# Performance work log

Measured on AMD Instinct MI355X. Metric: run time of the kernel, lower is better.

The kernel has to match this reference:

```python
import jax, jax.numpy as jnp
import numpy as np

HEADS = 8
DIM_HEAD = 64
SCALE = DIM_HEAD ** -0.5


def setup_inputs() -> dict:
    key = jax.random.key(0)
    ks = jax.random.split(key, 7)
    B, N, Dq = 2, 4096, 512
    M, Dc = 4096, 768
    inner = HEADS * DIM_HEAD  # 512
    x = jax.random.normal(ks[0], (B, N, Dq), dtype=jnp.float32)
    context = jax.random.normal(ks[1], (B, M, Dc), dtype=jnp.float32)
    # weights stored [in, out] (torch Linear weight transposed)
    Wq = jax.random.normal(ks[2], (Dq, inner), dtype=jnp.float32) * (Dq ** -0.5)
    Wk = jax.random.normal(ks[3], (Dc, inner), dtype=jnp.float32) * (Dc ** -0.5)
    Wv = jax.random.normal(ks[4], (Dc, inner), dtype=jnp.float32) * (Dc ** -0.5)
    Wo = jax.random.normal(ks[5], (inner, Dq), dtype=jnp.float32) * (inner ** -0.5)
    bo = jax.random.normal(ks[6], (Dq,), dtype=jnp.float32) * 0.01
    return {"x": x, "context": context, "Wq": Wq, "Wk": Wk, "Wv": Wv, "Wo": Wo, "bo": bo}


def reference(x, context, Wq, Wk, Wv, Wo, bo):
    B, N, _ = x.shape
    M = context.shape[1]
    h, d = HEADS, DIM_HEAD
    q = (x @ Wq).reshape(B, N, h, d)                      # b n h d
    k = ((context @ Wk) * SCALE).reshape(B, M, h, d)      # scale applied to k, as in source
    v = (context @ Wv).reshape(B, M, h, d)
    scores = jnp.einsum('bnhd,bmhd->bhnm', q, k)          # full QK^T
    attn = jax.nn.softmax(scores, axis=-1)
    out = jnp.einsum('bhnm,bmhd->bnhd', attn, v).reshape(B, N, h * d)
    return out @ Wo + bo  # dropout p=0.0 -> identity
```

## Files before the change

kernel.cpp:

```cpp
#include <hip/hip_runtime.h>

typedef unsigned short u16;
typedef __attribute__((ext_vector_type(4))) unsigned short u16x4;
typedef __attribute__((ext_vector_type(8))) unsigned short u16x8;
typedef __attribute__((ext_vector_type(8))) short s16x8;
typedef __attribute__((ext_vector_type(4))) float f32x4;
typedef __attribute__((ext_vector_type(16))) float f32x16;
typedef __attribute__((ext_vector_type(4))) unsigned int u32x4;

#define LOG2E 1.4426950408889634f

__device__ __forceinline__ u16 f2bf(float f) {
    return __builtin_bit_cast(unsigned short, static_cast<__bf16>(f));
}

__device__ __forceinline__ float fexp2(float x) {
#if __has_builtin(__builtin_amdgcn_exp2f)
    return __builtin_amdgcn_exp2f(x);
#else
    return exp2f(x);
#endif
}

__device__ __forceinline__ s16x8 ld_frag(const u16* p) {
    return __builtin_bit_cast(s16x8, *reinterpret_cast<const u16x8*>(p));
}

__device__ __forceinline__ f32x4 mfma16(s16x8 a, s16x8 b, f32x4 c) {
    return __builtin_amdgcn_mfma_f32_16x16x32_bf16(a, b, c, 0, 0, 0);
}

__device__ __forceinline__ f32x16 mfma32(s16x8 a, s16x8 b, f32x16 c) {
    return __builtin_amdgcn_mfma_f32_32x32x16_bf16(a, b, c, 0, 0, 0);
}

__device__ __forceinline__ unsigned cvt_pk_bf16(float lo, float hi2) {
    unsigned r;
    asm("v_cvt_pk_bf16_f32 %0, %1, %2" : "=v"(r) : "v"(lo), "v"(hi2));
    return r;
}

__device__ __forceinline__ void plane32_swap(unsigned& x, unsigned& y) {
#if __has_builtin(__builtin_amdgcn_permlane32_swap)
    auto r = __builtin_amdgcn_permlane32_swap(x, y, false, false);
    x = r[0];
    y = r[1];
#else
    asm("v_permlane32_swap_b32 %0, %1" : "+v"(x), "+v"(y));
#endif
}

__device__ __forceinline__ void async16(const u16* g, u16* lds) {
    __builtin_amdgcn_global_load_lds(
        (__attribute__((address_space(1))) void*)const_cast<u16*>(g),
        (__attribute__((address_space(3))) void*)lds, 16, 0, 0);
}

__global__ __launch_bounds__(256) void cvt_bf16_kernel(const float* __restrict__ in,
                                                       u16* __restrict__ out, int n8) {
    int i = blockIdx.x * 256 + threadIdx.x;
    if (i >= n8) return;
    const f32x4* p = (const f32x4*)in + ((size_t)i << 1);
    f32x4 a = p[0], c = p[1];
    u16x8 v;
    v[0] = f2bf(a[0]); v[1] = f2bf(a[1]); v[2] = f2bf(a[2]); v[3] = f2bf(a[3]);
    v[4] = f2bf(c[0]); v[5] = f2bf(c[1]); v[6] = f2bf(c[2]); v[7] = f2bf(c[3]);
    *((u16x8*)out + i) = v;
}

__global__ __launch_bounds__(256) void wtrans_kernel(const float* __restrict__ W,
                                                     u16* __restrict__ Wt, int Kd, float scale) {
    __shared__ float t[32][33];
    const int k0 = blockIdx.x << 5, n0 = blockIdx.y << 5;
    const int tx = threadIdx.x, ty = threadIdx.y;
#pragma unroll
    for (int i = 0; i < 32; i += 8)
        t[ty + i][tx] = W[(size_t)(k0 + ty + i) * 512 + n0 + tx] * scale;
    __syncthreads();
#pragma unroll
    for (int i = 0; i < 32; i += 8)
        Wt[(size_t)(n0 + ty + i) * Kd + k0 + tx] = f2bf(t[tx][ty + i]);
}

__global__ __launch_bounds__(256) void vtrans_kernel(const u16* __restrict__ Vb,
                                                     u16* __restrict__ Vt) {
    __shared__ u16 t[64][72];
    const int bh = blockIdx.y, m0 = blockIdx.x << 6;
    const int b = bh >> 3, h = bh & 7;
    const int tid = threadIdx.x;
#pragma unroll
    for (int i = 0; i < 2; i++) {
        int f = tid + i * 256, r = f >> 3, sg = f & 7;
        u16x8 v = *(const u16x8*)(Vb + (size_t)(b * 4096 + m0 + r) * 512 + (h << 6) + (sg << 3));
        *(u16x8*)&t[r][sg << 3] = v;
    }
    __syncthreads();
#pragma unroll
    for (int i = 0; i < 2; i++) {
        int f = tid + i * 256, dr = f >> 3, sg = f & 7;
        u16x8 v;
#pragma unroll
        for (int j = 0; j < 8; j++) v[j] = t[(sg << 3) + j][dr];
        *(u16x8*)(Vt + (size_t)bh * 262144 + (size_t)dr * 4096 + m0 + (sg << 3)) = v;
    }
}

template <bool BF16OUT>
__device__ __forceinline__ void gemm_body(const u16* __restrict__ A, const u16* __restrict__ Bt,
                                          void* __restrict__ Cv, const float* __restrict__ bias,
                                          int K) {
    __shared__ u16 Ab[2][128 * 64];
    __shared__ u16 Bb[2][128 * 64];
    const int tid = threadIdx.x;
    const int w = tid >> 6, l = tid & 63;
    const int lg = l >> 4, lq = l & 15;
    const int wm = w >> 1, wn = w & 1;
    const int bm = blockIdx.y, bn = blockIdx.x;
    const int KT = K >> 6;

    f32x4 acc[4][4];
#pragma unroll
    for (int i = 0; i < 4; i++)
#pragma unroll
        for (int j = 0; j < 4; j++) acc[i][j] = (f32x4){0.f, 0.f, 0.f, 0.f};

    const u16* Ag0 = A + (size_t)bm * 128 * K;
    const u16* Bg0 = Bt + (size_t)bn * 128 * K;
    const int srow = l >> 3, scol = (l & 7) << 3;

    auto stage = [&](int kt, int buf) {
#pragma unroll
        for (int i = 0; i < 4; i++) {
            const int c = (w << 2) + i;
            const int row = (c << 3) + srow;
            async16(Ag0 + (size_t)row * K + kt * 64 + scol, &Ab[buf][c << 9]);
            async16(Bg0 + (size_t)row * K + kt * 64 + scol, &Bb[buf][c << 9]);
        }
    };

    stage(0, 0);
    for (int kt = 0; kt < KT; ++kt) {
        __syncthreads();
        if (kt + 1 < KT) stage(kt + 1, (kt + 1) & 1);
        const u16* As = Ab[kt & 1];
        const u16* Bs = Bb[kt & 1];
#pragma unroll
        for (int s = 0; s < 2; s++) {
            s16x8 af[4], bfr[4];
#pragma unroll
            for (int mt = 0; mt < 4; mt++)
                af[mt] = ld_frag(As + ((wm << 6) + (mt << 4) + lq) * 64 + (s << 5) + (lg << 3));
#pragma unroll
            for (int nt = 0; nt < 4; nt++)
                bfr[nt] = ld_frag(Bs + ((wn << 6) + (nt << 4) + lq) * 64 + (s << 5) + (lg << 3));
#pragma unroll
            for (int mt = 0; mt < 4; mt++)
#pragma unroll
                for (int nt = 0; nt < 4; nt++)
                    acc[mt][nt] = mfma16(af[mt], bfr[nt], acc[mt][nt]);
        }
    }
    const int row0 = bm * 128 + (wm << 6);
    const int col0 = bn * 128 + (wn << 6);
    if (BF16OUT) {
        u16* C = (u16*)Cv;
#pragma unroll
        for (int mt = 0; mt < 4; mt++)
#pragma unroll
            for (int nt = 0; nt < 4; nt++)
#pragma unroll
                for (int r = 0; r < 4; r++)
                    C[(size_t)(row0 + (mt << 4) + (lg << 2) + r) * 512 + col0 + (nt << 4) + lq] =
                        f2bf(acc[mt][nt][r]);
    } else {
        float* C = (float*)Cv;
        float bv[4];
#pragma unroll
        for (int nt = 0; nt < 4; nt++) bv[nt] = bias[col0 + (nt << 4) + lq];
#pragma unroll
        for (int mt = 0; mt < 4; mt++)
#pragma unroll
            for (int nt = 0; nt < 4; nt++)
#pragma unroll
                for (int r = 0; r < 4; r++)
                    C[(size_t)(row0 + (mt << 4) + (lg << 2) + r) * 512 + col0 + (nt << 4) + lq] =
                        acc[mt][nt][r] + bv[nt];
    }
}

__global__ __launch_bounds__(256, 2) void proj_gemm_kernel(
    const u16* __restrict__ xb, const u16* __restrict__ cb, const u16* __restrict__ Wqt,
    const u16* __restrict__ Wkt, const u16* __restrict__ Wvt, u16* __restrict__ Qb,
    u16* __restrict__ Kb, u16* __restrict__ Vb) {
    const int z = blockIdx.z;
    if (z == 0)
        gemm_body<true>(xb, Wqt, Qb, nullptr, 512);
    else if (z == 1)
        gemm_body<true>(cb, Wkt, Kb, nullptr, 768);
    else
        gemm_body<true>(cb, Wvt, Vb, nullptr, 768);
}

__global__ __launch_bounds__(256, 2) void out_gemm_kernel(const u16* __restrict__ Ob,
                                                          const u16* __restrict__ Wot,
                                                          float* __restrict__ out,
                                                          const float* __restrict__ bias) {
    gemm_body<false>(Ob, Wot, out, bias, 512);
}

__global__ __launch_bounds__(256, 2) void attn_kernel(const u16* __restrict__ Qb,
                                                      const u16* __restrict__ Kb,
                                                      const u16* __restrict__ Vt,
                                                      u16* __restrict__ Ob) {
    __shared__ u16 Kl[2][64][64];
    __shared__ u16 Vl[2][64][64];
    __shared__ float xBuf[4][32];
    const int tid = threadIdx.x;
    const int w = tid >> 6, l = tid & 63;
    const int lq = l & 31, hi = l >> 5;
    const int bh = blockIdx.y, b = bh >> 3, h = bh & 7;
    const int q0 = (blockIdx.x << 7) + (w << 5);

    const u16* Qp = Qb + (size_t)(b * 4096 + q0 + lq) * 512 + (h << 6) + (hi << 3);
    s16x8 qf[4];
#pragma unroll
    for (int s = 0; s < 4; s++) qf[s] = ld_frag(Qp + (s << 4));

    const u16* Kg0 = Kb + (size_t)b * 4096 * 512 + (h << 6);
    const u16* Vg0 = Vt + (size_t)bh * 262144;

    const int srow = tid >> 3, sseg = tid & 7;
    const int swcol = (sseg ^ (srow & 7)) << 3;

    int offs[4];
    {
        const int clo = (hi ^ (l & 1)) << 3;
        const int d2 = (l >> 1) & 3;
#pragma unroll
        for (int s = 0; s < 4; s++) offs[s] = clo + ((s ^ d2) << 4);
    }

    f32x16 oacc[2];
#pragma unroll
    for (int dt = 0; dt < 2; dt++)
#pragma unroll
        for (int r = 0; r < 16; r++) oacc[dt][r] = 0.f;
    float m_st = -3.0e38f, l_st = 0.f;

    {
        u16x8 ka = *(const u16x8*)(Kg0 + (size_t)srow * 512 + sseg * 8);
        u16x8 kc = *(const u16x8*)(Kg0 + (size_t)(srow + 32) * 512 + sseg * 8);
        u16x8 va = *(const u16x8*)(Vg0 + (size_t)srow * 4096 + sseg * 8);
        u16x8 vc = *(const u16x8*)(Vg0 + (size_t)(srow + 32) * 4096 + sseg * 8);
        *(u16x8*)&Kl[0][srow][swcol] = ka;
        *(u16x8*)&Kl[0][srow + 32][swcol] = kc;
        *(u16x8*)&Vl[0][srow][swcol] = va;
        *(u16x8*)&Vl[0][srow + 32][swcol] = vc;
    }

    for (int it = 0; it < 64; ++it) {
        const int buf = it & 1;
        __syncthreads();
        u16x8 ka, kc, va, vc;
        const bool more = it + 1 < 64;
        if (more) {
            const int kv = (it + 1) << 6;
            ka = *(const u16x8*)(Kg0 + (size_t)(kv + srow) * 512 + sseg * 8);
            kc = *(const u16x8*)(Kg0 + (size_t)(kv + srow + 32) * 512 + sseg * 8);
            va = *(const u16x8*)(Vg0 + (size_t)srow * 4096 + kv + sseg * 8);
            vc = *(const u16x8*)(Vg0 + (size_t)(srow + 32) * 4096 + kv + sseg * 8);
        }
        const u16* Kbuf = &Kl[buf][0][0];
        const u16* Vbuf = &Vl[buf][0][0];

        f32x16 sacc[2];
#pragma unroll
        for (int t = 0; t < 2; t++) {
#pragma unroll
            for (int r = 0; r < 16; r++) sacc[t][r] = 0.f;
#pragma unroll
            for (int s = 0; s < 4; s++) {
                s16x8 kf = ld_frag(Kbuf + ((lq + (t << 5)) << 6) + offs[s]);
                sacc[t] = mfma32(kf, qf[s], sacc[t]);
            }
        }

        float pm = sacc[0][0];
#pragma unroll
        for (int t = 0; t < 2; t++)
#pragma unroll
            for (int r = 0; r < 16; r++) pm = fmaxf(pm, sacc[t][r]);
        pm = fmaxf(pm, __shfl_xor(pm, 32));
        const float mn = fmaxf(m_st, pm);
        const float alpha = fexp2(m_st - mn);
        m_st = mn;
        float rs = 0.f;
#pragma unroll
        for (int t = 0; t < 2; t++)
#pragma unroll
            for (int r = 0; r < 16; r++) {
                float p = fexp2(sacc[t][r] - mn);
                sacc[t][r] = p;
                rs += p;
            }
        rs += __shfl_xor(rs, 32);
        l_st = l_st * alpha + rs;

        if (hi == 0) xBuf[w][lq] = alpha;
        asm volatile("s_waitcnt lgkmcnt(0)" ::: "memory");
        __builtin_amdgcn_sched_barrier(0);
        f32x4 ar[4];
#pragma unroll
        for (int u = 0; u < 4; u++) ar[u] = *(const f32x4*)&xBuf[w][(hi << 2) + (u << 3)];
#pragma unroll
        for (int dt = 0; dt < 2; dt++)
#pragma unroll
            for (int r = 0; r < 16; r++) oacc[dt][r] *= ar[r >> 2][r & 3];

        s16x8 aw[4];
#pragma unroll
        for (int s = 0; s < 4; s++) {
            const int tt = s >> 1, base2 = (s & 1) << 3;
            unsigned X1 = cvt_pk_bf16(sacc[tt][base2 + 0], sacc[tt][base2 + 1]);
            unsigned Y1 = cvt_pk_bf16(sacc[tt][base2 + 4], sacc[tt][base2 + 5]);
            unsigned X2 = cvt_pk_bf16(sacc[tt][base2 + 2], sacc[tt][base2 + 3]);
            unsigned Y2 = cvt_pk_bf16(sacc[tt][base2 + 6], sacc[tt][base2 + 7]);
            plane32_swap(X1, Y1);
            plane32_swap(X2, Y2);
            u32x4 wv;
            wv[0] = X1; wv[1] = X2; wv[2] = Y1; wv[3] = Y2;
            aw[s] = __builtin_bit_cast(s16x8, wv);
        }

#pragma unroll
        for (int s = 0; s < 4; s++)
#pragma unroll
            for (int dt = 0; dt < 2; dt++) {
                s16x8 vf = ld_frag(Vbuf + ((lq + (dt << 5)) << 6) + offs[s]);
                oacc[dt] = mfma32(aw[s], vf, oacc[dt]);
            }

        if (more) {
            const int nb = buf ^ 1;
            *(u16x8*)&Kl[nb][srow][swcol] = ka;
            *(u16x8*)&Kl[nb][srow + 32][swcol] = kc;
            *(u16x8*)&Vl[nb][srow][swcol] = va;
            *(u16x8*)&Vl[nb][srow + 32][swcol] = vc;
        }
    }

    if (hi == 0) xBuf[w][lq] = 1.f / l_st;
    asm volatile("s_waitcnt lgkmcnt(0)" ::: "memory");
    __builtin_amdgcn_sched_barrier(0);
    f32x4 lr[4];
#pragma unroll
    for (int u = 0; u < 4; u++) lr[u] = *(const f32x4*)&xBuf[w][(hi << 2) + (u << 3)];
    u16* Op = Ob + (size_t)(b * 4096 + q0) * 512 + (h << 6);
#pragma unroll
    for (int dt = 0; dt < 2; dt++)
#pragma unroll
        for (int r = 0; r < 16; r++) {
            const int q = (r & 3) + ((r >> 2) << 3) + (hi << 2);
            Op[(size_t)q * 512 + lq + (dt << 5)] = f2bf(oacc[dt][r] * lr[r >> 2][r & 3]);
        }
}

extern "C" void kernel_launch(void* const* d_in, const int* in_sizes, int n_in, void* d_out,
                              int out_size, void* d_ws, size_t ws_size, hipStream_t stream) {
    const float* x = (const float*)d_in[0];
    const float* ctx = (const float*)d_in[1];
    const float* Wq = (const float*)d_in[2];
    const float* Wk = (const float*)d_in[3];
    const float* Wv = (const float*)d_in[4];
    const float* Wo = (const float*)d_in[5];
    const float* bo = (const float*)d_in[6];
    float* out = (float*)d_out;

    char* ws = (char*)d_ws;
    u16* xb  = (u16*)(ws);
    u16* cb  = (u16*)(ws + 8388608);
    u16* Wqt = (u16*)(ws + 20971520);
    u16* Wkt = (u16*)(ws + 21495808);
    u16* Wvt = (u16*)(ws + 22282240);
    u16* Wot = (u16*)(ws + 23068672);
    u16* Qb  = (u16*)(ws + 23592960);
    u16* Kb  = (u16*)(ws + 31981568);
    u16* Vb  = (u16*)(ws + 40370176);
    u16* Vt  = (u16*)(ws + 48758784);
    u16* Ob  = (u16*)(ws + 57147392);

    cvt_bf16_kernel<<<dim3(2048), dim3(256), 0, stream>>>(x, xb, 4194304 / 8);
    cvt_bf16_kernel<<<dim3(3072), dim3(256), 0, stream>>>(ctx, cb, 6291456 / 8);
    wtrans_kernel<<<dim3(16, 16), dim3(32, 8), 0, stream>>>(Wq, Wqt, 512, 1.0f);
    wtrans_kernel<<<dim3(24, 16), dim3(32, 8), 0, stream>>>(Wk, Wkt, 768, 0.125f * LOG2E);
    wtrans_kernel<<<dim3(24, 16), dim3(32, 8), 0, stream>>>(Wv, Wvt, 768, 1.0f);
    wtrans_kernel<<<dim3(16, 16), dim3(32, 8), 0, stream>>>(Wo, Wot, 512, 1.0f);
    proj_gemm_kernel<<<dim3(4, 64, 3), dim3(256), 0, stream>>>(xb, cb, Wqt, Wkt, Wvt, Qb, Kb, Vb);
    vtrans_kernel<<<dim3(64, 16), dim3(256), 0, stream>>>(Vb, Vt);
    attn_kernel<<<dim3(32, 16), dim3(256), 0, stream>>>(Qb, Kb, Vt, Ob);
    out_gemm_kernel<<<dim3(4, 64), dim3(256), 0, stream>>>(Ob, Wot, out, bo);
}
```

Before: 180.8 us.

## Restructure attention: 2-wave blocks, lazy rescale, MFMA row-sum, max3 reductions

```diff
diff --git a/kernel.cpp b/kernel.cpp
--- a/kernel.cpp
+++ b/kernel.cpp
@@ -20,6 +20,12 @@
 #else
     return exp2f(x);
 #endif
+}
+
+__device__ __forceinline__ float max3f(float a, float b, float c) {
+    float r;
+    asm("v_max3_f32 %0, %1, %2, %3" : "=v"(r) : "v"(a), "v"(b), "v"(c));
+    return r;
 }
 
 __device__ __forceinline__ s16x8 ld_frag(const u16* p) {
@@ -208,18 +214,18 @@
     gemm_body<false>(Ob, Wot, out, bias, 512);
 }
 
-__global__ __launch_bounds__(256, 2) void attn_kernel(const u16* __restrict__ Qb,
+__global__ __launch_bounds__(128, 2) void attn_kernel(const u16* __restrict__ Qb,
                                                       const u16* __restrict__ Kb,
                                                       const u16* __restrict__ Vt,
                                                       u16* __restrict__ Ob) {
     __shared__ u16 Kl[2][64][64];
     __shared__ u16 Vl[2][64][64];
-    __shared__ float xBuf[4][32];
+    __shared__ float xBuf[2][32];
     const int tid = threadIdx.x;
     const int w = tid >> 6, l = tid & 63;
     const int lq = l & 31, hi = l >> 5;
     const int bh = blockIdx.y, b = bh >> 3, h = bh & 7;
-    const int q0 = (blockIdx.x << 7) + (w << 5);
+    const int q0 = (blockIdx.x << 6) + (w << 5);
 
     const u16* Qp = Qb + (size_t)(b * 4096 + q0 + lq) * 512 + (h << 6) + (hi << 3);
     s16x8 qf[4];
@@ -231,6 +237,8 @@
 
     const int srow = tid >> 3, sseg = tid & 7;
     const int swcol = (sseg ^ (srow & 7)) << 3;
+    const u16* Kgp = Kg0 + (size_t)srow * 512 + (sseg << 3);
+    const u16* Vgp = Vg0 + (size_t)srow * 4096 + (sseg << 3);
 
     int offs[4];
     {
@@ -240,82 +248,91 @@
         for (int s = 0; s < 4; s++) offs[s] = clo + ((s ^ d2) << 4);
     }
 
-    f32x16 oacc[2];
-#pragma unroll
-    for (int dt = 0; dt < 2; dt++)
-#pragma unroll
-        for (int r = 0; r < 16; r++) oacc[dt][r] = 0.f;
-    float m_st = -3.0e38f, l_st = 0.f;
-
-    {
-        u16x8 ka = *(const u16x8*)(Kg0 + (size_t)srow * 512 + sseg * 8);
-        u16x8 kc = *(const u16x8*)(Kg0 + (size_t)(srow + 32) * 512 + sseg * 8);
-        u16x8 va = *(const u16x8*)(Vg0 + (size_t)srow * 4096 + sseg * 8);
-        u16x8 vc = *(const u16x8*)(Vg0 + (size_t)(srow + 32) * 4096 + sseg * 8);
-        *(u16x8*)&Kl[0][srow][swcol] = ka;
-        *(u16x8*)&Kl[0][srow + 32][swcol] = kc;
-        *(u16x8*)&Vl[0][srow][swcol] = va;
-        *(u16x8*)&Vl[0][srow + 32][swcol] = vc;
-    }
-
-    for (int it = 0; it < 64; ++it) {
-        const int buf = it & 1;
+    f32x16 oacc[2], ls;
+#pragma unroll
+    for (int r = 0; r < 16; r++) { oacc[0][r] = 0.f; oacc[1][r] = 0.f; ls[r] = 0.f; }
+    float m_st = -3.0e38f;
+
+    s16x8 onesb;
+#pragma unroll
+    for (int j = 0; j < 8; j++) onesb[j] = 0x3F80;
+
+#pragma unroll
+    for (int j = 0; j < 4; j++) {
+        u16x8 kv_ = *(const u16x8*)(Kgp + (size_t)(j << 4) * 512);
+        u16x8 vv_ = *(const u16x8*)(Vgp + (size_t)(j << 4) * 4096);
+        *(u16x8*)&Kl[0][srow + (j << 4)][swcol] = kv_;
+        *(u16x8*)&Vl[0][srow + (j << 4)][swcol] = vv_;
+    }
+
+    auto step = [&](const int buf, const int it) {
         __syncthreads();
-        u16x8 ka, kc, va, vc;
-        const bool more = it + 1 < 64;
+        u16x8 kpre[4], vpre[4];
+        const bool more = (it + 1) < 64;
         if (more) {
             const int kv = (it + 1) << 6;
-            ka = *(const u16x8*)(Kg0 + (size_t)(kv + srow) * 512 + sseg * 8);
-            kc = *(const u16x8*)(Kg0 + (size_t)(kv + srow + 32) * 512 + sseg * 8);
-            va = *(const u16x8*)(Vg0 + (size_t)srow * 4096 + kv + sseg * 8);
-            vc = *(const u16x8*)(Vg0 + (size_t)(srow + 32) * 4096 + kv + sseg * 8);
+#pragma unroll
+            for (int j = 0; j < 4; j++) {
+                kpre[j] = *(const u16x8*)(Kgp + (size_t)(kv + (j << 4)) * 512);
+                vpre[j] = *(const u16x8*)(Vgp + (size_t)(j << 4) * 4096 + kv);
+            }
         }
         const u16* Kbuf = &Kl[buf][0][0];
         const u16* Vbuf = &Vl[buf][0][0];
 
         f32x16 sacc[2];
 #pragma unroll
-        for (int t = 0; t < 2; t++) {
-#pragma unroll
-            for (int r = 0; r < 16; r++) sacc[t][r] = 0.f;
+        for (int r = 0; r < 16; r++) { sacc[0][r] = 0.f; sacc[1][r] = 0.f; }
+        __builtin_amdgcn_s_setprio(1);
+#pragma unroll
+        for (int t = 0; t < 2; t++)
 #pragma unroll
             for (int s = 0; s < 4; s++) {
                 s16x8 kf = ld_frag(Kbuf + ((lq + (t << 5)) << 6) + offs[s]);
                 sacc[t] = mfma32(kf, qf[s], sacc[t]);
             }
-        }
-
-        float pm = sacc[0][0];
+        __builtin_amdgcn_s_setprio(0);
+
+        float s1[11], s2[4];
+#pragma unroll
+        for (int i = 0; i < 10; i++) {
+            const int k0 = 3 * i;
+            float a = sacc[k0 >> 4][k0 & 15];
+            float c = sacc[(k0 + 1) >> 4][(k0 + 1) & 15];
+            float d = sacc[(k0 + 2) >> 4][(k0 + 2) & 15];
+            s1[i] = max3f(a, c, d);
+        }
+        s1[10] = fmaxf(sacc[1][14], sacc[1][15]);
+        s2[0] = max3f(s1[0], s1[1], s1[2]);
+        s2[1] = max3f(s1[3], s1[4], s1[5]);
+        s2[2] = max3f(s1[6], s1[7], s1[8]);
+        s2[3] = fmaxf(s1[9], s1[10]);
+        float pm = fmaxf(max3f(s2[0], s2[1], s2[2]), s2[3]);
+        pm = fmaxf(pm, __shfl_xor(pm, 32));
+
+        if (!__all(pm <= m_st + 8.0f)) {
+            const float mn = fmaxf(m_st, pm);
+            const float alpha = fexp2(m_st - mn);
+            m_st = mn;
+            if (hi == 0) xBuf[w][lq] = alpha;
+            asm volatile("s_waitcnt lgkmcnt(0)" ::: "memory");
+            __builtin_amdgcn_sched_barrier(0);
+            f32x4 ar[4];
+#pragma unroll
+            for (int u = 0; u < 4; u++) ar[u] = *(const f32x4*)&xBuf[w][(hi << 2) + (u << 3)];
+#pragma unroll
+            for (int r = 0; r < 16; r++) {
+                const float a = ar[r >> 2][r & 3];
+                oacc[0][r] *= a;
+                oacc[1][r] *= a;
+                ls[r] *= a;
+            }
+        }
+
 #pragma unroll
         for (int t = 0; t < 2; t++)
 #pragma unroll
-            for (int r = 0; r < 16; r++) pm = fmaxf(pm, sacc[t][r]);
-        pm = fmaxf(pm, __shfl_xor(pm, 32));
-        const float mn = fmaxf(m_st, pm);
-        const float alpha = fexp2(m_st - mn);
-        m_st = mn;
-        float rs = 0.f;
-#pragma unroll
-        for (int t = 0; t < 2; t++)
-#pragma unroll
-            for (int r = 0; r < 16; r++) {
-                float p = fexp2(sacc[t][r] - mn);
-                sacc[t][r] = p;
-                rs += p;
-            }
-        rs += __shfl_xor(rs, 32);
-        l_st = l_st * alpha + rs;
-
-        if (hi == 0) xBuf[w][lq] = alpha;
-        asm volatile("s_waitcnt lgkmcnt(0)" ::: "memory");
-        __builtin_amdgcn_sched_barrier(0);
-        f32x4 ar[4];
-#pragma unroll
-        for (int u = 0; u < 4; u++) ar[u] = *(const f32x4*)&xBuf[w][(hi << 2) + (u << 3)];
-#pragma unroll
-        for (int dt = 0; dt < 2; dt++)
-#pragma unroll
-            for (int r = 0; r < 16; r++) oacc[dt][r] *= ar[r >> 2][r & 3];
+            for (int r = 0; r < 16; r++) sacc[t][r] = fexp2(sacc[t][r] - m_st);
 
         s16x8 aw[4];
 #pragma unroll
@@ -332,37 +349,41 @@
             aw[s] = __builtin_bit_cast(s16x8, wv);
         }
 
-#pragma unroll
-        for (int s = 0; s < 4; s++)
+        __builtin_amdgcn_s_setprio(1);
+#pragma unroll
+        for (int s = 0; s < 4; s++) {
+            ls = mfma32(aw[s], onesb, ls);
 #pragma unroll
             for (int dt = 0; dt < 2; dt++) {
                 s16x8 vf = ld_frag(Vbuf + ((lq + (dt << 5)) << 6) + offs[s]);
                 oacc[dt] = mfma32(aw[s], vf, oacc[dt]);
             }
+        }
+        __builtin_amdgcn_s_setprio(0);
 
         if (more) {
             const int nb = buf ^ 1;
-            *(u16x8*)&Kl[nb][srow][swcol] = ka;
-            *(u16x8*)&Kl[nb][srow + 32][swcol] = kc;
-            *(u16x8*)&Vl[nb][srow][swcol] = va;
-            *(u16x8*)&Vl[nb][srow + 32][swcol] = vc;
-        }
-    }
-
-    if (hi == 0) xBuf[w][lq] = 1.f / l_st;
-    asm volatile("s_waitcnt lgkmcnt(0)" ::: "memory");
-    __builtin_amdgcn_sched_barrier(0);
-    f32x4 lr[4];
-#pragma unroll
-    for (int u = 0; u < 4; u++) lr[u] = *(const f32x4*)&xBuf[w][(hi << 2) + (u << 3)];
+#pragma unroll
+            for (int j = 0; j < 4; j++) {
+                *(u16x8*)&Kl[nb][srow + (j << 4)][swcol] = kpre[j];
+                *(u16x8*)&Vl[nb][srow + (j << 4)][swcol] = vpre[j];
+            }
+        }
+    };
+
+    for (int i2 = 0; i2 < 32; ++i2) {
+        step(0, i2 * 2);
+        step(1, i2 * 2 + 1);
+    }
+
     u16* Op = Ob + (size_t)(b * 4096 + q0) * 512 + (h << 6);
 #pragma unroll
-    for (int dt = 0; dt < 2; dt++)
-#pragma unroll
-        for (int r = 0; r < 16; r++) {
-            const int q = (r & 3) + ((r >> 2) << 3) + (hi << 2);
-            Op[(size_t)q * 512 + lq + (dt << 5)] = f2bf(oacc[dt][r] * lr[r >> 2][r & 3]);
-        }
+    for (int r = 0; r < 16; r++) {
+        const float li = 1.f / ls[r];
+        const int q = (r & 3) + ((r >> 2) << 3) + (hi << 2);
+        Op[(size_t)q * 512 + lq] = f2bf(oacc[0][r] * li);
+        Op[(size_t)q * 512 + lq + 32] = f2bf(oacc[1][r] * li);
+    }
 }
 
 extern "C" void kernel_launch(void* const* d_in, const int* in_sizes, int n_in, void* d_out,
@@ -397,6 +418,6 @@
     wtrans_kernel<<<dim3(16, 16), dim3(32, 8), 0, stream>>>(Wo, Wot, 512, 1.0f);
     proj_gemm_kernel<<<dim3(4, 64, 3), dim3(256), 0, stream>>>(xb, cb, Wqt, Wkt, Wvt, Qb, Kb, Vb);
     vtrans_kernel<<<dim3(64, 16), dim3(256), 0, stream>>>(Vb, Vt);
-    attn_kernel<<<dim3(32, 16), dim3(256), 0, stream>>>(Qb, Kb, Vt, Ob);
+    attn_kernel<<<dim3(64, 16), dim3(128), 0, stream>>>(Qb, Kb, Vt, Ob);
     out_gemm_kernel<<<dim3(4, 64), dim3(256), 0, stream>>>(Ob, Wot, out, bo);
 }
```

New measurement: 184.9 us. 1.02x slower.
